# Kernel optimization log

Hardware: AMD Instinct MI355X
Metric: run time of the kernel (lower is better)

Reference implementation:

```python
import jax, jax.numpy as jnp
import numpy as np

NUM_BOXES = 16384
NUM_CLASS = 3
CODE_SIZE = 7
NMS_PRE = 1024
NMS_POST = 512
NMS_THRESH = 0.8
EPS = 1e-8


def _cross(a, b):
    return a[..., 0] * b[..., 1] - a[..., 1] * b[..., 0]


def _bev_corners(b5):
    # b5: (..., 5) = (cx, cy, dx, dy, ry) -> corners (..., 4, 2)
    c, s = jnp.cos(b5[..., 4]), jnp.sin(b5[..., 4])
    off = jnp.array([[0.5, 0.5], [-0.5, 0.5], [-0.5, -0.5], [0.5, -0.5]], dtype=b5.dtype)
    lx = b5[..., 2:3] * off[:, 0]  # (..., 4)
    ly = b5[..., 3:4] * off[:, 1]
    cx = b5[..., 0:1] + lx * c[..., None] - ly * s[..., None]
    cy = b5[..., 1:2] + lx * s[..., None] + ly * c[..., None]
    return jnp.stack([cx, cy], axis=-1)


def _points_in_box(p, b5):
    # p: (..., K, 2), b5: (..., 5) -> (..., K) bool (point inside rotated rect)
    c, s = jnp.cos(b5[..., 4:5]), jnp.sin(b5[..., 4:5])
    rel = p - b5[..., None, 0:2]
    qx = rel[..., 0] * c + rel[..., 1] * s
    qy = -rel[..., 0] * s + rel[..., 1] * c
    return (jnp.abs(qx) <= b5[..., 2:3] * 0.5 + 1e-5) & (jnp.abs(qy) <= b5[..., 3:4] * 0.5 + 1e-5)


def _pairwise_bev_iou(b5):
    # b5: (N, 5) -> (N, N) rotated BEV IoU (matches iou3d nms_gpu's BEV IoU)
    a = b5[:, None, :]
    b = b5[None, :, :]
    ca = _bev_corners(a)  # (N,1,4,2)
    cb = _bev_corners(b)  # (1,N,4,2)
    # edge-edge segment intersections: (N,N,4,4)
    a0, da = ca, jnp.roll(ca, -1, axis=-2) - ca
    b0, db = cb, jnp.roll(cb, -1, axis=-2) - cb
    A0, DA = a0[..., :, None, :], da[..., :, None, :]
    B0, DB = b0[..., None, :, :], db[..., None, :, :]
    den = _cross(DA, DB)
    d = B0 - A0
    den_s = jnp.where(jnp.abs(den) > EPS, den, 1.0)
    t = _cross(d, DB) / den_s
    u = _cross(d, DA) / den_s
    ok = (jnp.abs(den) > EPS) & (t >= 0) & (t <= 1) & (u >= 0) & (u <= 1)
    p_ee = A0 + t[..., None] * DA  # (N,N,4,4,2)
    shp = p_ee.shape[:-3]
    p_ee = p_ee.reshape(shp + (16, 2))
    ok = ok.reshape(shp + (16,))
    in_b = _points_in_box(ca, b)  # corners of A inside B: (N,N,4)
    in_a = _points_in_box(cb, a)  # corners of B inside A: (N,N,4)
    pts = jnp.concatenate([p_ee,
                           jnp.broadcast_to(ca, shp + (4, 2)),
                           jnp.broadcast_to(cb, shp + (4, 2))], axis=-2)  # (N,N,24,2)
    msk = jnp.concatenate([ok, in_b, in_a], axis=-1)  # (N,N,24)
    # order candidate vertices by angle around centroid (intersection is convex)
    cnt = jnp.maximum(msk.sum(-1, keepdims=True), 1)
    ctr = (pts * msk[..., None]).sum(-2, keepdims=True) / cnt[..., None]  # (N,N,1,2)
    ang = jnp.arctan2(pts[..., 1] - ctr[..., 1], pts[..., 0] - ctr[..., 0])
    ang = jnp.where(msk, ang, 1e9)  # invalid points sorted to the end
    order = jnp.argsort(ang, axis=-1)
    pts_s = jnp.take_along_axis(pts, order[..., None], axis=-2)
    msk_s = jnp.take_along_axis(msk, order, axis=-1)
    first = pts_s[..., 0:1, :]
    poly = jnp.where(msk_s[..., None], pts_s, first)  # pad with first vertex (zero shoelace contribution)
    inter = 0.5 * jnp.abs(_cross(poly, jnp.roll(poly, -1, axis=-2)).sum(-1))
    area_a = a[..., 2] * a[..., 3]
    area_b = b[..., 2] * b[..., 3]
    return inter / jnp.maximum(area_a + area_b - inter, 1e-6)


def _greedy_nms(iou, thresh):
    n = iou.shape[0]
    idx = jnp.arange(n)

    def body(i, supp):
        alive = jnp.logical_not(supp[i])
        return supp | (alive & (iou[i] > thresh) & (idx > i))

    supp = jax.lax.fori_loop(0, n, body, jnp.zeros((n,), dtype=bool))
    return ~supp


def _select_one(box_preds, cls_preds):
    # box_preds: (M, 7), cls_preds: (M, C) -> padded selected indices + validity
    scores = jnp.max(cls_preds, axis=1)
    _, top_idx = jax.lax.top_k(scores, NMS_PRE)  # score-descending, like torch.topk
    bev = box_preds[top_idx][:, jnp.array([0, 1, 3, 4, 6])]  # (cx,cy,dx,dy,ry)
    iou = _pairwise_bev_iou(bev)
    keep = _greedy_nms(iou, NMS_THRESH)
    pri = jnp.where(keep, jnp.arange(NMS_PRE), 2 * NMS_PRE)
    pos = jnp.sort(pri)[:NMS_POST]  # kept positions in score order
    valid = pos < NMS_PRE
    sel = top_idx[jnp.minimum(pos, NMS_PRE - 1)]
    return sel, valid


def setup_inputs() -> dict:
    key = jax.random.key(0)
    k1, k2, k3, k4, k5 = jax.random.split(key, 5)
    B = 2
    xy = jax.random.uniform(k1, (B, NUM_BOXES, 2), minval=-50.0, maxval=50.0)
    z = jax.random.uniform(k2, (B, NUM_BOXES, 1), minval=-2.0, maxval=1.0)
    dims = jax.random.uniform(k3, (B, NUM_BOXES, 3), minval=1.0, maxval=5.0)
    ry = jax.random.uniform(k4, (B, NUM_BOXES, 1), minval=-np.pi, maxval=np.pi)
    batch_box_preds = jnp.concatenate([xy, z, dims, ry], axis=-1).astype(jnp.float32)
    batch_cls_preds = (jax.random.normal(k5, (B, NUM_BOXES, NUM_CLASS)) * 3.0).astype(jnp.float32)
    return {"batch_box_preds": batch_box_preds, "batch_cls_preds": batch_cls_preds}


def reference(batch_box_preds, batch_cls_preds):
    # RoIHeadTemplate.proposal_layer: per-sample max-score, class-agnostic NMS,
    # scatter into zero-padded (B, NMS_POST, ...) tensors.
    sel, valid = jax.vmap(_select_one)(batch_box_preds, batch_cls_preds)  # (B, NMS_POST)
    rois = jnp.take_along_axis(batch_box_preds, sel[..., None], axis=1)
    logits = jnp.take_along_axis(batch_cls_preds, sel[..., None], axis=1)
    labels = jnp.argmax(logits, axis=-1)
    scores = jnp.max(logits, axis=-1)
    v = valid[..., None]
    rois = jnp.where(v, rois, 0.0)
    logits = jnp.where(v, logits, 0.0)
    scores = jnp.where(valid, scores, 0.0)
    roi_labels = jnp.where(valid, labels, 0) + 1  # padded slots end up as 1, same as torch (zeros + 1)
    return rois, scores, roi_labels, logits
```

## Files before the change

### kernel.cpp

```cpp
#include <hip/hip_runtime.h>
#include <hip/hip_bf16.h>
#include <math.h>

#define NBOX   16384
#define NPRE   1024
#define NPOST  512
#define NMS_TH 0.8f
#define DEN_EPS 1e-8f
#define NCAND  2048
#define NBUCK  8192

typedef unsigned long long ull;

__device__ __forceinline__ unsigned mono_f32(float a) {
  unsigned u = __float_as_uint(a);
  return (u & 0x80000000u) ? ~u : (u | 0x80000000u);
}

__global__ __launch_bounds__(1024) void k_hist(
    const float* __restrict__ cls, ull* __restrict__ cand,
    unsigned* __restrict__ candCount, unsigned* __restrict__ nz) {
  __shared__ unsigned hist[NBUCK];
  __shared__ unsigned wsuf[16];
  __shared__ unsigned thrT;
  __shared__ unsigned cnt;
  int b = blockIdx.x;
  int t = threadIdx.x;
  int lane = t & 63, wv = t >> 6;
  nz[b * NPRE + t] = 0u;
#pragma unroll
  for (int k = 0; k < NBUCK / 1024; ++k) hist[t + k * 1024] = 0u;
  if (t == 0) cnt = 0u;
  __syncthreads();

  ull key[16];
#pragma unroll
  for (int k = 0; k < 16; ++k) {
    int i = k * 1024 + t;
    const float* cc = cls + ((size_t)b * NBOX + i) * 3;
    float s = fmaxf(cc[0], fmaxf(cc[1], cc[2]));
    unsigned u = mono_f32(s);
    key[k] = ((ull)u << 14) | (ull)(16383 - i);
    atomicAdd(&hist[u >> 19], 1u);
  }
  __syncthreads();

  unsigned s8 = 0;
#pragma unroll
  for (int k = 0; k < 8; ++k) s8 += hist[t * 8 + k];
  unsigned v = s8;
#pragma unroll
  for (int off = 1; off < 64; off <<= 1) {
    unsigned o = __shfl_down(v, off, 64);
    if (lane + off < 64) v += o;
  }
  if (lane == 0) wsuf[wv] = v;
  __syncthreads();
  if (t < 16) {
    unsigned x = wsuf[t];
#pragma unroll
    for (int off = 1; off < 16; off <<= 1) {
      unsigned o = __shfl_down(x, off, 64);
      if (t + off < 16) x += o;
    }
    wsuf[t] = x;
  }
  __syncthreads();
  unsigned Sown = v + ((wv < 15) ? wsuf[wv + 1] : 0u);
  unsigned Snxt = Sown - s8;
  if (Sown >= NPRE && Snxt < NPRE) {
    unsigned c = Snxt;
    unsigned T = t * 8;
    for (int k = 7; k >= 0; --k) {
      c += hist[t * 8 + k];
      if (c >= NPRE) { T = t * 8 + k; break; }
    }
    thrT = T;
  }
  __syncthreads();
  unsigned T = thrT;
#pragma unroll
  for (int k = 0; k < 16; ++k) {
    bool c = (unsigned)(key[k] >> 33) >= T;
    ull bal = __ballot(c);
    if (bal) {
      unsigned base = 0;
      if (lane == 0) base = atomicAdd(&cnt, (unsigned)__popcll(bal));
      base = (unsigned)__shfl((int)base, 0, 64);
      if (c) {
        unsigned pos = base + (unsigned)__popcll(bal & ((1ull << lane) - 1ull));
        if (pos < NCAND) cand[(size_t)b * NCAND + pos] = key[k];
      }
    }
  }
  __syncthreads();
  if (t == 0) candCount[b] = (cnt < NCAND) ? cnt : NCAND;
}

__global__ __launch_bounds__(256) void k_ranksel(
    const float* __restrict__ box, const ull* __restrict__ cand,
    const unsigned* __restrict__ candCount,
    int* __restrict__ topi, float* __restrict__ binfo, float4* __restrict__ pinfo) {
  __shared__ ull lk[NCAND];
  int b = blockIdx.y;
  int tid = threadIdx.x;
  int j = blockIdx.x * 256 + tid;
  unsigned C = candCount[b];
#pragma unroll
  for (int k = 0; k < NCAND / 256; ++k) {
    int idx = k * 256 + tid;
    lk[idx] = ((unsigned)idx < C) ? cand[(size_t)b * NCAND + idx] : 0ULL;
  }
  __syncthreads();
  ull my = ((unsigned)j < C) ? lk[j] : 0ULL;
  int r = 0;
  const ulonglong2* p2 = (const ulonglong2*)lk;
#pragma unroll 8
  for (int k = 0; k < NCAND / 2; ++k) {
    ulonglong2 kk = p2[k];
    r += (kk.x > my) ? 1 : 0;
    r += (kk.y > my) ? 1 : 0;
  }
  if ((unsigned)j >= C || r >= NPRE) return;
  int i = 16383 - (int)(my & 0x3FFFULL);
  topi[b * NPRE + r] = i;
  const float* bp = box + ((size_t)b * NBOX + i) * 7;
  float x = bp[0], y = bp[1], dx = bp[3], dy = bp[4], ry = bp[6];
  float c = cosf(ry), s = sinf(ry);
  float* o = binfo + ((size_t)b * NPRE + r) * 16;
  o[0] = x; o[1] = y; o[2] = dx; o[3] = dy; o[4] = c; o[5] = s;
  const float offx[4] = {0.5f, -0.5f, -0.5f, 0.5f};
  const float offy[4] = {0.5f, 0.5f, -0.5f, -0.5f};
#pragma unroll
  for (int k = 0; k < 4; ++k) {
    float lx = dx * offx[k], ly = dy * offy[k];
    o[6 + k]  = x + lx * c - ly * s;
    o[10 + k] = y + lx * s + ly * c;
  }
  float rad = 0.5f * sqrtf(dx * dx + dy * dy);
  float area = dx * dy;
  o[14] = rad; o[15] = area;
  pinfo[(size_t)b * NPRE + r] = make_float4(x, y, rad, area);
}

__device__ bool iou_exact_gt(const float* __restrict__ Ab, const float* __restrict__ Bb) {
  float ax = Ab[0], ay = Ab[1], bx = Bb[0], by = Bb[1];
  float aA = Ab[15], aB = Bb[15];
  float acx[4], acy[4], bcx[4], bcy[4];
#pragma unroll
  for (int k = 0; k < 4; ++k) {
    acx[k] = Ab[6 + k]; acy[k] = Ab[10 + k];
    bcx[k] = Bb[6 + k]; bcy[k] = Bb[10 + k];
  }
  float px[24], py[24];
  bool act[24];
#pragma unroll
  for (int p = 0; p < 4; ++p) {
    float A0x = acx[p], A0y = acy[p];
    float DAx = acx[(p + 1) & 3] - A0x, DAy = acy[(p + 1) & 3] - A0y;
#pragma unroll
    for (int q = 0; q < 4; ++q) {
      float B0x = bcx[q], B0y = bcy[q];
      float DBx = bcx[(q + 1) & 3] - B0x, DBy = bcy[(q + 1) & 3] - B0y;
      float den = DAx * DBy - DAy * DBx;
      float dxx = B0x - A0x, dyy = B0y - A0y;
      bool dok = fabsf(den) > DEN_EPS;
      float dens = dok ? den : 1.0f;
      float t = (dxx * DBy - dyy * DBx) / dens;
      float u = (dxx * DAy - dyy * DAx) / dens;
      int k = p * 4 + q;
      px[k] = A0x + t * DAx;
      py[k] = A0y + t * DAy;
      act[k] = dok && t >= 0.f && t <= 1.f && u >= 0.f && u <= 1.f;
    }
  }
  float cA = Ab[4], sA = Ab[5], cB = Bb[4], sB = Bb[5];
#pragma unroll
  for (int k = 0; k < 4; ++k) {
    float rx = acx[k] - bx, ry = acy[k] - by;
    float qx =  rx * cB + ry * sB, qy = -rx * sB + ry * cB;
    px[16 + k] = acx[k]; py[16 + k] = acy[k];
    act[16 + k] = (fabsf(qx) <= Bb[2] * 0.5f + 1e-5f) && (fabsf(qy) <= Bb[3] * 0.5f + 1e-5f);
  }
#pragma unroll
  for (int k = 0; k < 4; ++k) {
    float rx = bcx[k] - ax, ry = bcy[k] - ay;
    float qx =  rx * cA + ry * sA, qy = -rx * sA + ry * cA;
    px[20 + k] = bcx[k]; py[20 + k] = bcy[k];
    act[20 + k] = (fabsf(qx) <= Ab[2] * 0.5f + 1e-5f) && (fabsf(qy) <= Ab[3] * 0.5f + 1e-5f);
  }
  int cnt = 0; float sx = 0.f, sy = 0.f;
#pragma unroll
  for (int k = 0; k < 24; ++k)
    if (act[k]) { cnt++; sx += px[k]; sy += py[k]; }
  float fc = (float)(cnt > 1 ? cnt : 1);
  float cx0 = sx / fc, cy0 = sy / fc;
  ull key[24];
#pragma unroll
  for (int k = 0; k < 24; ++k) {
    float ang = atan2f(py[k] - cy0, px[k] - cx0);
    key[k] = act[k] ? ((((ull)mono_f32(ang)) << 5) | (ull)k) : ~0ull;
  }
  ull kmin = ~0ull; float fx = 0.f, fy = 0.f;
#pragma unroll
  for (int k = 0; k < 24; ++k) {
    bool lt = key[k] < kmin;
    kmin = lt ? key[k] : kmin;
    fx = lt ? px[k] : fx;
    fy = lt ? py[k] : fy;
  }
  float ssum = 0.f;
#pragma unroll
  for (int k = 0; k < 24; ++k) {
    ull myk = key[k];
    ull best = ~0ull; float nx = fx, ny = fy;
#pragma unroll
    for (int j = 0; j < 24; ++j) {
      bool c = (key[j] > myk) && (key[j] < best);
      best = c ? key[j] : best;
      nx = c ? px[j] : nx;
      ny = c ? py[j] : ny;
    }
    float contrib = px[k] * ny - py[k] * nx;
    ssum += (myk != ~0ull) ? contrib : 0.f;
  }
  float inter = 0.5f * fabsf(ssum);
  float uni = aA + aB - inter;
  return inter / fmaxf(uni, 1e-6f) > NMS_TH;
}

__global__ __launch_bounds__(256) void k_pairs(
    const float* __restrict__ binfo, const float4* __restrict__ pinfo,
    ull* __restrict__ mask, unsigned* __restrict__ nz) {
  int wv = (blockIdx.x * 256 + threadIdx.x) >> 6;
  int lane = threadIdx.x & 63;
  int w = wv & 15;
  int i = (wv >> 4) & (NPRE - 1);
  int b = wv >> 14;
  if (w * 64 + 63 <= i) return;
  int j = w * 64 + lane;
  float4 pj = pinfo[(size_t)b * NPRE + j];
  float4 pi = pinfo[(size_t)b * NPRE + i];
  bool cand = false;
  if (j > i) {
    float ddx = pi.x - pj.x, ddy = pi.y - pj.y;
    float rr = pi.z + pj.z + 1e-3f;
    if (ddx * ddx + ddy * ddy <= rr * rr) {
      float mn = fminf(pi.w, pj.w), mx = fmaxf(pi.w, pj.w);
      if (mn > NMS_TH * mx) cand = true;
    }
  }
  const float* base = binfo + (size_t)b * NPRE * 16;
  bool pred = cand && iou_exact_gt(base + (size_t)i * 16, base + (size_t)j * 16);
  ull bal = __ballot(pred);
  if (lane == 0 && bal) {
    mask[((size_t)b * NPRE + i) * 16 + w] = bal;
    atomicOr(&nz[b * NPRE + i], 1u << w);
  }
}

__global__ __launch_bounds__(1024) void k_final(
    const float* __restrict__ box, const float* __restrict__ cls,
    const int* __restrict__ topi, const ull* __restrict__ mask,
    const unsigned* __restrict__ nz, float* __restrict__ out, int B) {
  __shared__ ull remv_sh[16];
  int b = blockIdx.x;
  int p = threadIdx.x;
  int lane = p & 63, wid = p >> 6;

  if (wid == 0) {
    ull rfr[16];
#pragma unroll
    for (int w = 0; w < 16; ++w) {
      unsigned vz = nz[b * NPRE + w * 64 + lane];
      rfr[w] = __ballot(vz != 0u);
    }
    ull remv = 0;
    for (int w = 0; w < 16; ++w) {
      ull bb = rfr[w];
      while (bb) {
        int ii = __ffsll(bb) - 1;
        bb &= bb - 1;
        int row = w * 64 + ii;
        ull rw = __shfl(remv, w, 64);
        if (!((rw >> ii) & 1ULL)) {
          unsigned nzi = nz[b * NPRE + row];
          ull m = 0;
          if (lane < 16 && ((nzi >> lane) & 1u))
            m = mask[((size_t)b * NPRE + row) * 16 + lane];
          remv |= m;
        }
      }
    }
    if (lane < 16) remv_sh[lane] = remv;
  }
  __syncthreads();

  ull rw = remv_sh[wid];
  int alive = ((rw >> lane) & 1ULL) ? 0 : 1;
  int v = alive;
#pragma unroll
  for (int off = 1; off < 64; off <<= 1) {
    int t = __shfl_up(v, off, 64);
    if (lane >= off) v += t;
  }
  __shared__ int wtot[16], woff[17];
  if (lane == 63) wtot[wid] = v;
  __syncthreads();
  if (p == 0) {
    int acc = 0;
    for (int t = 0; t < 16; ++t) { woff[t] = acc; acc += wtot[t]; }
    woff[16] = acc;
  }
  __syncthreads();
  int excl = v - alive + woff[wid];
  int total = woff[16];
  float* rois   = out;
  float* scores = out + (size_t)B * NPOST * 7;
  float* labels = scores + (size_t)B * NPOST;
  float* logits = labels + (size_t)B * NPOST;
  if (alive && excl < NPOST) {
    int s = excl;
    int orig = topi[b * NPRE + p];
    const float* bb = box + ((size_t)b * NBOX + orig) * 7;
    float* ro = rois + ((size_t)b * NPOST + s) * 7;
#pragma unroll
    for (int c = 0; c < 7; ++c) ro[c] = bb[c];
    const float* cc = cls + ((size_t)b * NBOX + orig) * 3;
    float l0 = cc[0], l1 = cc[1], l2 = cc[2];
    float m = fmaxf(l0, fmaxf(l1, l2));
    int lab = (l0 == m) ? 0 : ((l1 == m) ? 1 : 2);
    scores[b * NPOST + s] = m;
    labels[b * NPOST + s] = (float)(lab + 1);
    float* lg = logits + ((size_t)b * NPOST + s) * 3;
    lg[0] = l0; lg[1] = l1; lg[2] = l2;
  }
  if (p < NPOST && p >= total) {
    float* ro = rois + ((size_t)b * NPOST + p) * 7;
#pragma unroll
    for (int c = 0; c < 7; ++c) ro[c] = 0.f;
    scores[b * NPOST + p] = 0.f;
    labels[b * NPOST + p] = 1.f;
    float* lg = logits + ((size_t)b * NPOST + p) * 3;
    lg[0] = 0.f; lg[1] = 0.f; lg[2] = 0.f;
  }
}

extern "C" void kernel_launch(void* const* d_in, const int* in_sizes, int n_in,
                              void* d_out, int out_size, void* d_ws, size_t ws_size,
                              hipStream_t stream) {
  const float* box = (const float*)d_in[0];
  const float* cls = (const float*)d_in[1];
  float* out = (float*)d_out;
  int B = in_sizes[0] / (NBOX * 7);

  char* w = (char*)d_ws;
  size_t off = 0;
  ull* cand        = (ull*)(w + off);      off += (size_t)B * NCAND * sizeof(ull);
  unsigned* candCt = (unsigned*)(w + off); off += (size_t)B * sizeof(unsigned);
  int* topi        = (int*)(w + off);      off += (size_t)B * NPRE * sizeof(int);
  off = (off + 63) & ~(size_t)63;
  float* binfo     = (float*)(w + off);    off += (size_t)B * NPRE * 16 * sizeof(float);
  float4* pinfo    = (float4*)(w + off);   off += (size_t)B * NPRE * sizeof(float4);
  ull* mask        = (ull*)(w + off);      off += (size_t)B * NPRE * 16 * sizeof(ull);
  unsigned* nz     = (unsigned*)(w + off); off += (size_t)B * NPRE * sizeof(unsigned);
  (void)off; (void)ws_size; (void)out_size; (void)n_in;

  hipLaunchKernelGGL(k_hist,    dim3(B), dim3(1024), 0, stream, cls, cand, candCt, nz);
  hipLaunchKernelGGL(k_ranksel, dim3(NCAND / 256, B), dim3(256), 0, stream, box, cand, candCt, topi, binfo, pinfo);
  hipLaunchKernelGGL(k_pairs,   dim3(B * NPRE * 16 / 4), dim3(256), 0, stream, binfo, pinfo, mask, nz);
  hipLaunchKernelGGL(k_final,   dim3(B), dim3(1024), 0, stream, box, cls, topi, mask, nz, out, B);
}
```

Before: 157.7 us.

## Fuse pipeline into one cooperative kernel with compacted IoU worklist

Replaces the four separate launches (histogram top-k, rank select, pairwise IoU, NMS gather) with a single cooperative kernel separated by grid-wide syncs, with the histogram spread across the whole grid. The pairwise stage first does the cheap circle and area prefilter, then compacts the surviving (i, j) pairs into a global worklist, so the expensive exact IoU runs densely instead of inside divergent wavefronts. The final stage prefetches mask rows for suppressing boxes into shared memory in parallel before the serial suppression scan. This removes launch gaps and IoU divergence, at the cost of several grid barriers, a fixed 256-block grid that assumes a small batch, and worklist capacity limits.

New measurement: 291.5 us. 84.9% more time.

```diff
diff --git a/kernel.cpp b/kernel.cpp
--- a/kernel.cpp
+++ b/kernel.cpp
@@ -1,6 +1,8 @@
 #include <hip/hip_runtime.h>
-#include <hip/hip_bf16.h>
+#include <hip/hip_cooperative_groups.h>
 #include <math.h>
+
+namespace cg = cooperative_groups;
 
 #define NBOX   16384
 #define NPRE   1024
@@ -9,138 +11,16 @@
 #define DEN_EPS 1e-8f
 #define NCAND  2048
 #define NBUCK  8192
+#define GRIDB  256
+#define BLK    256
+#define WMAX   (1u << 20)
+#define ROWCAP 128
 
 typedef unsigned long long ull;
 
 __device__ __forceinline__ unsigned mono_f32(float a) {
   unsigned u = __float_as_uint(a);
   return (u & 0x80000000u) ? ~u : (u | 0x80000000u);
-}
-
-__global__ __launch_bounds__(1024) void k_hist(
-    const float* __restrict__ cls, ull* __restrict__ cand,
-    unsigned* __restrict__ candCount, unsigned* __restrict__ nz) {
-  __shared__ unsigned hist[NBUCK];
-  __shared__ unsigned wsuf[16];
-  __shared__ unsigned thrT;
-  __shared__ unsigned cnt;
-  int b = blockIdx.x;
-  int t = threadIdx.x;
-  int lane = t & 63, wv = t >> 6;
-  nz[b * NPRE + t] = 0u;
-#pragma unroll
-  for (int k = 0; k < NBUCK / 1024; ++k) hist[t + k * 1024] = 0u;
-  if (t == 0) cnt = 0u;
-  __syncthreads();
-
-  ull key[16];
-#pragma unroll
-  for (int k = 0; k < 16; ++k) {
-    int i = k * 1024 + t;
-    const float* cc = cls + ((size_t)b * NBOX + i) * 3;
-    float s = fmaxf(cc[0], fmaxf(cc[1], cc[2]));
-    unsigned u = mono_f32(s);
-    key[k] = ((ull)u << 14) | (ull)(16383 - i);
-    atomicAdd(&hist[u >> 19], 1u);
-  }
-  __syncthreads();
-
-  unsigned s8 = 0;
-#pragma unroll
-  for (int k = 0; k < 8; ++k) s8 += hist[t * 8 + k];
-  unsigned v = s8;
-#pragma unroll
-  for (int off = 1; off < 64; off <<= 1) {
-    unsigned o = __shfl_down(v, off, 64);
-    if (lane + off < 64) v += o;
-  }
-  if (lane == 0) wsuf[wv] = v;
-  __syncthreads();
-  if (t < 16) {
-    unsigned x = wsuf[t];
-#pragma unroll
-    for (int off = 1; off < 16; off <<= 1) {
-      unsigned o = __shfl_down(x, off, 64);
-      if (t + off < 16) x += o;
-    }
-    wsuf[t] = x;
-  }
-  __syncthreads();
-  unsigned Sown = v + ((wv < 15) ? wsuf[wv + 1] : 0u);
-  unsigned Snxt = Sown - s8;
-  if (Sown >= NPRE && Snxt < NPRE) {
-    unsigned c = Snxt;
-    unsigned T = t * 8;
-    for (int k = 7; k >= 0; --k) {
-      c += hist[t * 8 + k];
-      if (c >= NPRE) { T = t * 8 + k; break; }
-    }
-    thrT = T;
-  }
-  __syncthreads();
-  unsigned T = thrT;
-#pragma unroll
-  for (int k = 0; k < 16; ++k) {
-    bool c = (unsigned)(key[k] >> 33) >= T;
-    ull bal = __ballot(c);
-    if (bal) {
-      unsigned base = 0;
-      if (lane == 0) base = atomicAdd(&cnt, (unsigned)__popcll(bal));
-      base = (unsigned)__shfl((int)base, 0, 64);
-      if (c) {
-        unsigned pos = base + (unsigned)__popcll(bal & ((1ull << lane) - 1ull));
-        if (pos < NCAND) cand[(size_t)b * NCAND + pos] = key[k];
-      }
-    }
-  }
-  __syncthreads();
-  if (t == 0) candCount[b] = (cnt < NCAND) ? cnt : NCAND;
-}
-
-__global__ __launch_bounds__(256) void k_ranksel(
-    const float* __restrict__ box, const ull* __restrict__ cand,
-    const unsigned* __restrict__ candCount,
-    int* __restrict__ topi, float* __restrict__ binfo, float4* __restrict__ pinfo) {
-  __shared__ ull lk[NCAND];
-  int b = blockIdx.y;
-  int tid = threadIdx.x;
-  int j = blockIdx.x * 256 + tid;
-  unsigned C = candCount[b];
-#pragma unroll
-  for (int k = 0; k < NCAND / 256; ++k) {
-    int idx = k * 256 + tid;
-    lk[idx] = ((unsigned)idx < C) ? cand[(size_t)b * NCAND + idx] : 0ULL;
-  }
-  __syncthreads();
-  ull my = ((unsigned)j < C) ? lk[j] : 0ULL;
-  int r = 0;
-  const ulonglong2* p2 = (const ulonglong2*)lk;
-#pragma unroll 8
-  for (int k = 0; k < NCAND / 2; ++k) {
-    ulonglong2 kk = p2[k];
-    r += (kk.x > my) ? 1 : 0;
-    r += (kk.y > my) ? 1 : 0;
-  }
-  if ((unsigned)j >= C || r >= NPRE) return;
-  int i = 16383 - (int)(my & 0x3FFFULL);
-  topi[b * NPRE + r] = i;
-  const float* bp = box + ((size_t)b * NBOX + i) * 7;
-  float x = bp[0], y = bp[1], dx = bp[3], dy = bp[4], ry = bp[6];
-  float c = cosf(ry), s = sinf(ry);
-  float* o = binfo + ((size_t)b * NPRE + r) * 16;
-  o[0] = x; o[1] = y; o[2] = dx; o[3] = dy; o[4] = c; o[5] = s;
-  const float offx[4] = {0.5f, -0.5f, -0.5f, 0.5f};
-  const float offy[4] = {0.5f, 0.5f, -0.5f, -0.5f};
-#pragma unroll
-  for (int k = 0; k < 4; ++k) {
-    float lx = dx * offx[k], ly = dy * offy[k];
-    o[6 + k]  = x + lx * c - ly * s;
-    o[10 + k] = y + lx * s + ly * c;
-  }
-  float rad = 0.5f * sqrtf(dx * dx + dy * dy);
-  float area = dx * dy;
-  o[14] = rad; o[15] = area;
-  pinfo[(size_t)b * NPRE + r] = make_float4(x, y, rad, area);
 }
 
 __device__ bool iou_exact_gt(const float* __restrict__ Ab, const float* __restrict__ Bb) {
@@ -229,145 +109,340 @@
   return inter / fmaxf(uni, 1e-6f) > NMS_TH;
 }
 
-__global__ __launch_bounds__(256) void k_pairs(
-    const float* __restrict__ binfo, const float4* __restrict__ pinfo,
-    ull* __restrict__ mask, unsigned* __restrict__ nz) {
-  int wv = (blockIdx.x * 256 + threadIdx.x) >> 6;
-  int lane = threadIdx.x & 63;
-  int w = wv & 15;
-  int i = (wv >> 4) & (NPRE - 1);
-  int b = wv >> 14;
-  if (w * 64 + 63 <= i) return;
-  int j = w * 64 + lane;
-  float4 pj = pinfo[(size_t)b * NPRE + j];
-  float4 pi = pinfo[(size_t)b * NPRE + i];
-  bool cand = false;
-  if (j > i) {
-    float ddx = pi.x - pj.x, ddy = pi.y - pj.y;
-    float rr = pi.z + pj.z + 1e-3f;
-    if (ddx * ddx + ddy * ddy <= rr * rr) {
-      float mn = fminf(pi.w, pj.w), mx = fmaxf(pi.w, pj.w);
-      if (mn > NMS_TH * mx) cand = true;
-    }
-  }
-  const float* base = binfo + (size_t)b * NPRE * 16;
-  bool pred = cand && iou_exact_gt(base + (size_t)i * 16, base + (size_t)j * 16);
-  ull bal = __ballot(pred);
-  if (lane == 0 && bal) {
-    mask[((size_t)b * NPRE + i) * 16 + w] = bal;
-    atomicOr(&nz[b * NPRE + i], 1u << w);
-  }
-}
-
-__global__ __launch_bounds__(1024) void k_final(
-    const float* __restrict__ box, const float* __restrict__ cls,
-    const int* __restrict__ topi, const ull* __restrict__ mask,
-    const unsigned* __restrict__ nz, float* __restrict__ out, int B) {
+struct Params {
+  const float* box; const float* cls; float* out;
+  ull* keys; unsigned* hist; ull* cand; unsigned* candCnt;
+  int* topi; float* binfo; float4* pinfo; ull* mask; unsigned* nz;
+  unsigned* wl; unsigned* wcnt; unsigned wcap; int B;
+};
+
+__global__ __launch_bounds__(BLK) void k_all(Params P) {
+  cg::grid_group grid = cg::this_grid();
+  const int tid = threadIdx.x;
+  const int bid = blockIdx.x;
+  const int gid = bid * BLK + tid;
+  const int lane = tid & 63;
+  const int wv = tid >> 6;
+  const int B = P.B;
+  const int nkeys = B * NBOX;
+
+  __shared__ ull lk[NCAND];
+  __shared__ unsigned smallu[16];
   __shared__ ull remv_sh[16];
-  int b = blockIdx.x;
-  int p = threadIdx.x;
-  int lane = p & 63, wid = p >> 6;
-
-  if (wid == 0) {
+  __shared__ unsigned rlist[ROWCAP];
+  __shared__ unsigned rn_sh;
+
+  for (int x = gid; x < B * NBUCK; x += GRIDB * BLK) P.hist[x] = 0u;
+  for (int x = gid; x < B * NPRE; x += GRIDB * BLK) P.nz[x] = 0u;
+  if (gid < B) P.candCnt[gid] = 0u;
+  if (gid == B) P.wcnt[0] = 0u;
+  grid.sync();
+
+  if (gid < nkeys) {
+    const float* cc = P.cls + (size_t)gid * 3;
+    float s = fmaxf(cc[0], fmaxf(cc[1], cc[2]));
+    unsigned u = mono_f32(s);
+    int i = gid & (NBOX - 1);
+    int b = gid >> 14;
+    P.keys[gid] = ((ull)u << 14) | (ull)(16383 - i);
+    atomicAdd(&P.hist[b * NBUCK + (u >> 19)], 1u);
+  }
+  grid.sync();
+
+  if (gid < nkeys) {
+    int b = gid >> 14;
+    const unsigned* hb = P.hist + b * NBUCK;
+    unsigned csum = 0;
+#pragma unroll 8
+    for (int k = 0; k < 32; ++k) csum += hb[tid * 32 + k];
+    unsigned v = csum;
+#pragma unroll
+    for (int off = 1; off < 64; off <<= 1) {
+      unsigned o = __shfl_down((int)v, off, 64);
+      if (lane + off < 64) v += o;
+    }
+    if (lane == 0) smallu[wv] = v;
+    __syncthreads();
+    unsigned shi = 0;
+    for (int w2 = wv + 1; w2 < 4; ++w2) shi += smallu[w2];
+    unsigned incl = v + shi;
+    unsigned safter = incl - csum;
+    if (safter < NPRE && incl >= NPRE) {
+      unsigned c = safter;
+      for (int k = 31; k >= 0; --k) {
+        c += hb[tid * 32 + k];
+        if (c >= NPRE) { smallu[8] = (unsigned)(tid * 32 + k); break; }
+      }
+    }
+    __syncthreads();
+    unsigned T = smallu[8];
+    ull key = P.keys[gid];
+    bool c = (unsigned)(key >> 33) >= T;
+    ull bal = __ballot(c);
+    if (bal) {
+      unsigned base = 0;
+      if (lane == 0) base = atomicAdd(&P.candCnt[b], (unsigned)__popcll(bal));
+      base = (unsigned)__shfl((int)base, 0, 64);
+      if (c) {
+        unsigned pos = base + (unsigned)__popcll(bal & ((1ull << lane) - 1ull));
+        if (pos < NCAND) P.cand[(size_t)b * NCAND + pos] = key;
+      }
+    }
+  }
+  grid.sync();
+
+  if (bid < B * 8) {
+    int b = bid >> 3;
+    int j = (bid & 7) * BLK + tid;
+    unsigned C = P.candCnt[b]; if (C > NCAND) C = NCAND;
+#pragma unroll
+    for (int k = 0; k < NCAND / BLK; ++k) {
+      int idx = k * BLK + tid;
+      lk[idx] = ((unsigned)idx < C) ? P.cand[(size_t)b * NCAND + idx] : 0ULL;
+    }
+    __syncthreads();
+    ull my = ((unsigned)j < C) ? lk[j] : 0ULL;
+    int r = 0;
+    const ulonglong2* p2 = (const ulonglong2*)lk;
+#pragma unroll 8
+    for (int k = 0; k < NCAND / 2; ++k) {
+      ulonglong2 kk = p2[k];
+      r += (kk.x > my) ? 1 : 0;
+      r += (kk.y > my) ? 1 : 0;
+    }
+    if ((unsigned)j < C && r < NPRE) {
+      int i = 16383 - (int)(my & 0x3FFFULL);
+      P.topi[b * NPRE + r] = i;
+      const float* bp = P.box + ((size_t)b * NBOX + i) * 7;
+      float x = bp[0], y = bp[1], dx = bp[3], dy = bp[4], ry = bp[6];
+      float cth = cosf(ry), sth = sinf(ry);
+      float* o = P.binfo + ((size_t)b * NPRE + r) * 16;
+      o[0] = x; o[1] = y; o[2] = dx; o[3] = dy; o[4] = cth; o[5] = sth;
+      const float offx[4] = {0.5f, -0.5f, -0.5f, 0.5f};
+      const float offy[4] = {0.5f, 0.5f, -0.5f, -0.5f};
+#pragma unroll
+      for (int k = 0; k < 4; ++k) {
+        float lx = dx * offx[k], ly = dy * offy[k];
+        o[6 + k]  = x + lx * cth - ly * sth;
+        o[10 + k] = y + lx * sth + ly * cth;
+      }
+      float rad = 0.5f * sqrtf(dx * dx + dy * dy);
+      float area = dx * dy;
+      o[14] = rad; o[15] = area;
+      P.pinfo[(size_t)b * NPRE + r] = make_float4(x, y, rad, area);
+    }
+  }
+  grid.sync();
+
+  {
+    int nwords = B * NPRE * 16;
+    for (int wt = bid * (BLK / 64) + wv; wt < nwords; wt += GRIDB * (BLK / 64)) {
+      int w = wt & 15;
+      int i = (wt >> 4) & (NPRE - 1);
+      int b = wt >> 14;
+      if (w * 64 + 63 <= i) continue;
+      int j = w * 64 + lane;
+      float4 pj = P.pinfo[(size_t)b * NPRE + j];
+      float4 pi = P.pinfo[(size_t)b * NPRE + i];
+      bool cnd = false;
+      if (j > i) {
+        float ddx = pi.x - pj.x, ddy = pi.y - pj.y;
+        float rr = pi.z + pj.z + 1e-3f;
+        if (ddx * ddx + ddy * ddy <= rr * rr) {
+          float mn = fminf(pi.w, pj.w), mx = fmaxf(pi.w, pj.w);
+          if (mn > NMS_TH * mx) cnd = true;
+        }
+      }
+      ull bal = __ballot(cnd);
+      if (!bal) continue;
+      unsigned base = 0;
+      if (lane == 0) {
+        P.mask[((size_t)b * NPRE + i) * 16 + w] = 0ull;
+        base = atomicAdd(P.wcnt, (unsigned)__popcll(bal));
+      }
+      base = (unsigned)__shfl((int)base, 0, 64);
+      if (cnd) {
+        unsigned off = base + (unsigned)__popcll(bal & ((1ull << lane) - 1ull));
+        if (off < P.wcap)
+          P.wl[off] = ((unsigned)b << 20) | ((unsigned)i << 10) | (unsigned)j;
+      }
+    }
+  }
+  grid.sync();
+
+  {
+    unsigned n = P.wcnt[0];
+    if (n > P.wcap) n = P.wcap;
+    for (unsigned e = (unsigned)gid; e < n; e += GRIDB * BLK) {
+      unsigned pk = P.wl[e];
+      unsigned b = pk >> 20, i = (pk >> 10) & 1023, j = pk & 1023;
+      const float* base = P.binfo + (size_t)b * NPRE * 16;
+      if (iou_exact_gt(base + (size_t)i * 16, base + (size_t)j * 16)) {
+        atomicOr(&P.mask[((size_t)b * NPRE + i) * 16 + (j >> 6)], 1ull << (j & 63));
+        atomicOr(&P.nz[b * NPRE + i], 1u << (j >> 6));
+      }
+    }
+  }
+  grid.sync();
+
+  if (bid < B) {
+    int b = bid;
     ull rfr[16];
-#pragma unroll
-    for (int w = 0; w < 16; ++w) {
-      unsigned vz = nz[b * NPRE + w * 64 + lane];
-      rfr[w] = __ballot(vz != 0u);
-    }
-    ull remv = 0;
-    for (int w = 0; w < 16; ++w) {
-      ull bb = rfr[w];
-      while (bb) {
-        int ii = __ffsll(bb) - 1;
-        bb &= bb - 1;
-        int row = w * 64 + ii;
+    if (wv == 0) {
+#pragma unroll
+      for (int w = 0; w < 16; ++w) {
+        unsigned vz = P.nz[b * NPRE + w * 64 + lane];
+        rfr[w] = __ballot(vz != 0u);
+      }
+      if (lane == 0) {
+        unsigned n = 0;
+        for (int w = 0; w < 16; ++w) {
+          ull bb = rfr[w];
+          while (bb) {
+            int ii = __ffsll(bb) - 1;
+            bb &= bb - 1;
+            if (n < ROWCAP) rlist[n] = (unsigned)(w * 64 + ii);
+            n++;
+          }
+        }
+        rn_sh = n;
+      }
+    }
+    __syncthreads();
+    unsigned rn = rn_sh;
+    unsigned rpf = rn < ROWCAP ? rn : ROWCAP;
+    for (unsigned s = (unsigned)(tid >> 4); s < rpf; s += BLK / 16) {
+      unsigned row = rlist[s];
+      int wd = tid & 15;
+      unsigned nzi = P.nz[b * NPRE + row];
+      lk[s * 16 + wd] = ((nzi >> wd) & 1u)
+                        ? P.mask[((size_t)b * NPRE + row) * 16 + wd] : 0ull;
+    }
+    __syncthreads();
+    if (wv == 0) {
+      ull remv = 0;
+      for (unsigned s = 0; s < rn; ++s) {
+        unsigned row;
+        ull m;
+        if (s < ROWCAP) {
+          row = rlist[s];
+          m = (lane < 16) ? lk[s * 16 + lane] : 0ull;
+        } else {
+          unsigned cnt2 = 0; row = 0;
+          for (int w = 0; w < 16 && cnt2 <= s; ++w) {
+            ull bb = __ballot(P.nz[b * NPRE + w * 64 + lane] != 0u);
+            unsigned pc = (unsigned)__popcll(bb);
+            if (cnt2 + pc > s) {
+              unsigned need = s - cnt2;
+              ull t2 = bb;
+              for (unsigned q = 0; q < need; ++q) t2 &= t2 - 1;
+              row = w * 64 + (__ffsll(t2) - 1);
+              cnt2 = s + 1; break;
+            }
+            cnt2 += pc;
+          }
+          unsigned nzi = P.nz[b * NPRE + row];
+          m = (lane < 16 && ((nzi >> lane) & 1u))
+              ? P.mask[((size_t)b * NPRE + row) * 16 + lane] : 0ull;
+        }
+        int w = row >> 6, ii = row & 63;
         ull rw = __shfl(remv, w, 64);
-        if (!((rw >> ii) & 1ULL)) {
-          unsigned nzi = nz[b * NPRE + row];
-          ull m = 0;
-          if (lane < 16 && ((nzi >> lane) & 1u))
-            m = mask[((size_t)b * NPRE + row) * 16 + lane];
-          remv |= m;
-        }
-      }
-    }
-    if (lane < 16) remv_sh[lane] = remv;
-  }
-  __syncthreads();
-
-  ull rw = remv_sh[wid];
-  int alive = ((rw >> lane) & 1ULL) ? 0 : 1;
-  int v = alive;
-#pragma unroll
-  for (int off = 1; off < 64; off <<= 1) {
-    int t = __shfl_up(v, off, 64);
-    if (lane >= off) v += t;
-  }
-  __shared__ int wtot[16], woff[17];
-  if (lane == 63) wtot[wid] = v;
-  __syncthreads();
-  if (p == 0) {
-    int acc = 0;
-    for (int t = 0; t < 16; ++t) { woff[t] = acc; acc += wtot[t]; }
-    woff[16] = acc;
-  }
-  __syncthreads();
-  int excl = v - alive + woff[wid];
-  int total = woff[16];
-  float* rois   = out;
-  float* scores = out + (size_t)B * NPOST * 7;
-  float* labels = scores + (size_t)B * NPOST;
-  float* logits = labels + (size_t)B * NPOST;
-  if (alive && excl < NPOST) {
-    int s = excl;
-    int orig = topi[b * NPRE + p];
-    const float* bb = box + ((size_t)b * NBOX + orig) * 7;
-    float* ro = rois + ((size_t)b * NPOST + s) * 7;
-#pragma unroll
-    for (int c = 0; c < 7; ++c) ro[c] = bb[c];
-    const float* cc = cls + ((size_t)b * NBOX + orig) * 3;
-    float l0 = cc[0], l1 = cc[1], l2 = cc[2];
-    float m = fmaxf(l0, fmaxf(l1, l2));
-    int lab = (l0 == m) ? 0 : ((l1 == m) ? 1 : 2);
-    scores[b * NPOST + s] = m;
-    labels[b * NPOST + s] = (float)(lab + 1);
-    float* lg = logits + ((size_t)b * NPOST + s) * 3;
-    lg[0] = l0; lg[1] = l1; lg[2] = l2;
-  }
-  if (p < NPOST && p >= total) {
-    float* ro = rois + ((size_t)b * NPOST + p) * 7;
-#pragma unroll
-    for (int c = 0; c < 7; ++c) ro[c] = 0.f;
-    scores[b * NPOST + p] = 0.f;
-    labels[b * NPOST + p] = 1.f;
-    float* lg = logits + ((size_t)b * NPOST + p) * 3;
-    lg[0] = 0.f; lg[1] = 0.f; lg[2] = 0.f;
+        if (!((rw >> ii) & 1ULL)) remv |= m;
+      }
+      if (lane < 16) remv_sh[lane] = remv;
+    }
+    __syncthreads();
+
+    int p0 = tid * 4;
+    ull rw = remv_sh[p0 >> 6];
+    int a0 = !((rw >> ((p0 + 0) & 63)) & 1ULL);
+    int a1 = !((rw >> ((p0 + 1) & 63)) & 1ULL);
+    int a2 = !((rw >> ((p0 + 2) & 63)) & 1ULL);
+    int a3 = !((rw >> ((p0 + 3) & 63)) & 1ULL);
+    int myc = a0 + a1 + a2 + a3;
+    int v = myc;
+#pragma unroll
+    for (int off = 1; off < 64; off <<= 1) {
+      int t2 = __shfl_up(v, off, 64);
+      if (lane >= off) v += t2;
+    }
+    if (lane == 63) smallu[wv] = (unsigned)v;
+    __syncthreads();
+    int pre = 0;
+    for (int w2 = 0; w2 < wv; ++w2) pre += (int)smallu[w2];
+    int total = (int)(smallu[0] + smallu[1] + smallu[2] + smallu[3]);
+    int s = pre + v - myc;
+
+    float* rois   = P.out;
+    float* scores = P.out + (size_t)B * NPOST * 7;
+    float* labels = scores + (size_t)B * NPOST;
+    float* logits = labels + (size_t)B * NPOST;
+    int aa[4] = {a0, a1, a2, a3};
+#pragma unroll
+    for (int k = 0; k < 4; ++k) {
+      if (aa[k] && s < NPOST) {
+        int orig = P.topi[b * NPRE + p0 + k];
+        const float* bb = P.box + ((size_t)b * NBOX + orig) * 7;
+        float* ro = rois + ((size_t)b * NPOST + s) * 7;
+#pragma unroll
+        for (int c2 = 0; c2 < 7; ++c2) ro[c2] = bb[c2];
+        const float* cc = P.cls + ((size_t)b * NBOX + orig) * 3;
+        float l0 = cc[0], l1 = cc[1], l2 = cc[2];
+        float m = fmaxf(l0, fmaxf(l1, l2));
+        int lab = (l0 == m) ? 0 : ((l1 == m) ? 1 : 2);
+        scores[b * NPOST + s] = m;
+        labels[b * NPOST + s] = (float)(lab + 1);
+        float* lg = logits + ((size_t)b * NPOST + s) * 3;
+        lg[0] = l0; lg[1] = l1; lg[2] = l2;
+      }
+      s += aa[k];
+    }
+    for (int p2 = tid; p2 < NPOST; p2 += BLK) {
+      if (p2 >= total) {
+        float* ro = rois + ((size_t)b * NPOST + p2) * 7;
+#pragma unroll
+        for (int c2 = 0; c2 < 7; ++c2) ro[c2] = 0.f;
+        scores[b * NPOST + p2] = 0.f;
+        labels[b * NPOST + p2] = 1.f;
+        float* lg = logits + ((size_t)b * NPOST + p2) * 3;
+        lg[0] = 0.f; lg[1] = 0.f; lg[2] = 0.f;
+      }
+    }
   }
 }
 
 extern "C" void kernel_launch(void* const* d_in, const int* in_sizes, int n_in,
                               void* d_out, int out_size, void* d_ws, size_t ws_size,
                               hipStream_t stream) {
-  const float* box = (const float*)d_in[0];
-  const float* cls = (const float*)d_in[1];
-  float* out = (float*)d_out;
   int B = in_sizes[0] / (NBOX * 7);
 
   char* w = (char*)d_ws;
   size_t off = 0;
-  ull* cand        = (ull*)(w + off);      off += (size_t)B * NCAND * sizeof(ull);
-  unsigned* candCt = (unsigned*)(w + off); off += (size_t)B * sizeof(unsigned);
-  int* topi        = (int*)(w + off);      off += (size_t)B * NPRE * sizeof(int);
+  Params P;
+  P.box = (const float*)d_in[0];
+  P.cls = (const float*)d_in[1];
+  P.out = (float*)d_out;
+  P.B = B;
+  P.keys    = (ull*)(w + off);      off += (size_t)B * NBOX * sizeof(ull);
+  P.hist    = (unsigned*)(w + off); off += (size_t)B * NBUCK * sizeof(unsigned);
+  P.cand    = (ull*)(w + off);      off += (size_t)B * NCAND * sizeof(ull);
+  P.candCnt = (unsigned*)(w + off); off += 64;
+  P.topi    = (int*)(w + off);      off += (size_t)B * NPRE * sizeof(int);
   off = (off + 63) & ~(size_t)63;
-  float* binfo     = (float*)(w + off);    off += (size_t)B * NPRE * 16 * sizeof(float);
-  float4* pinfo    = (float4*)(w + off);   off += (size_t)B * NPRE * sizeof(float4);
-  ull* mask        = (ull*)(w + off);      off += (size_t)B * NPRE * 16 * sizeof(ull);
-  unsigned* nz     = (unsigned*)(w + off); off += (size_t)B * NPRE * sizeof(unsigned);
-  (void)off; (void)ws_size; (void)out_size; (void)n_in;
-
-  hipLaunchKernelGGL(k_hist,    dim3(B), dim3(1024), 0, stream, cls, cand, candCt, nz);
-  hipLaunchKernelGGL(k_ranksel, dim3(NCAND / 256, B), dim3(256), 0, stream, box, cand, candCt, topi, binfo, pinfo);
-  hipLaunchKernelGGL(k_pairs,   dim3(B * NPRE * 16 / 4), dim3(256), 0, stream, binfo, pinfo, mask, nz);
-  hipLaunchKernelGGL(k_final,   dim3(B), dim3(1024), 0, stream, box, cls, topi, mask, nz, out, B);
+  P.binfo   = (float*)(w + off);    off += (size_t)B * NPRE * 16 * sizeof(float);
+  P.pinfo   = (float4*)(w + off);   off += (size_t)B * NPRE * sizeof(float4);
+  P.mask    = (ull*)(w + off);      off += (size_t)B * NPRE * 16 * sizeof(ull);
+  P.nz      = (unsigned*)(w + off); off += (size_t)B * NPRE * sizeof(unsigned);
+  P.wcnt    = (unsigned*)(w + off); off += 64;
+  P.wl      = (unsigned*)(w + off);
+  unsigned wcap = 0;
+  if (ws_size > off) {
+    size_t rem = (ws_size - off) / sizeof(unsigned);
+    wcap = (rem < (size_t)WMAX) ? (unsigned)rem : WMAX;
+  }
+  P.wcap = wcap;
+  (void)out_size; (void)n_in;
+
+  void* args[] = {&P};
+  hipLaunchCooperativeKernel((void*)k_all, dim3(GRIDB), dim3(BLK), args, 0, stream);
 }
```
